# Performance work log

Hardware: AMD Instinct MI355X
Metric: run time of the kernel (lower is better)

The kernel has to match this reference:

```python
import jax, jax.numpy as jnp
import numpy as np

N = 20000        # nodes
NHID = 128       # hidden channels per head
HEADS = 4
E = 320000       # edges (before self-loops)
NLAYERS = 4
NCLASS = 40
DT, ALPHA, GAMMA = 1.0, 1.0, 1.0
NEG_SLOPE = 0.2  # PyG GATConv default


def setup_inputs() -> dict:
    key = jax.random.key(0)
    ks = jax.random.split(key, 8)
    s = 1.0 / np.sqrt(NHID)
    x = jax.random.normal(ks[0], (N, NHID), jnp.float32)
    src = jax.random.randint(ks[1], (E,), 0, N, dtype=jnp.int32)
    dst = jax.random.randint(ks[2], (E,), 0, N, dtype=jnp.int32)
    W = jax.random.normal(ks[3], (NHID, HEADS * NHID), jnp.float32) * s
    att_src = jax.random.normal(ks[4], (HEADS, NHID), jnp.float32) * s
    att_dst = jax.random.normal(ks[5], (HEADS, NHID), jnp.float32) * s
    bias = jnp.zeros((HEADS * NHID,), jnp.float32)
    Wr = jax.random.normal(ks[6], (NCLASS, NHID), jnp.float32) * s
    br = jnp.zeros((NCLASS,), jnp.float32)
    return {"x": x, "src": src, "dst": dst, "W": W, "att_src": att_src,
            "att_dst": att_dst, "bias": bias, "Wr": Wr, "br": br}


def reference(x, src, dst, W, att_src, att_dst, bias, Wr, br):
    # add self loops (PyG GATConv default)
    loop = jnp.arange(N, dtype=src.dtype)
    s_idx = jnp.concatenate([src, loop])
    d_idx = jnp.concatenate([dst, loop])

    def gat(X):
        # X: [N, NHID] -> out: [N, HEADS*NHID] (head-major, as PyG concat)
        h = (X @ W).reshape(N, HEADS, NHID)                  # [N,H,C]
        a_s = jnp.einsum('nhc,hc->nh', h, att_src)            # [N,H]
        a_d = jnp.einsum('nhc,hc->nh', h, att_dst)            # [N,H]
        e = jax.nn.leaky_relu(a_s[s_idx] + a_d[d_idx], NEG_SLOPE)  # [Etot,H]
        m = jax.ops.segment_max(e, d_idx, num_segments=N)     # scatter-softmax
        ex = jnp.exp(e - m[d_idx])
        den = jax.ops.segment_sum(ex, d_idx, num_segments=N)
        alpha = ex / den[d_idx]                               # [Etot,H]
        msg = h[s_idx] * alpha[..., None]                     # [Etot,H,C]
        out = jax.ops.segment_sum(msg, d_idx, num_segments=N)  # [N,H,C]
        return out.reshape(N, HEADS * NHID) + bias

    def step(carry, _):
        X, Y = carry
        # view(N, -1, nheads).mean(-1) on head-major [N, H*C] layout
        agg = jax.nn.elu(gat(X)).reshape(N, NHID, HEADS).mean(axis=-1)
        Y2 = Y + DT * (agg - ALPHA * Y - GAMMA * X)
        X2 = X + DT * Y2
        return (X2, Y2), (X2, Y2)

    (Xf, Yf), (Xs, Ys) = jax.lax.scan(step, (x, x), None, length=NLAYERS)
    X_all = jnp.concatenate([x[:, None], jnp.moveaxis(Xs, 0, 1)], axis=1)  # [N,L+1,C]
    Y_all = jnp.concatenate([x[:, None], jnp.moveaxis(Ys, 0, 1)], axis=1)
    out = Xf @ Wr.T + br                                     # [N, NCLASS]
    return out, X_all, Y_all
```

## Files before the change

kernel.cpp:

```cpp
#include <hip/hip_runtime.h>

typedef unsigned short u16;
typedef unsigned int u32;

#define N_NODES 20000
#define NE 320000
#define NLAYERS 4
#define NCLASS 40
#define NEG_SLOPE 0.2f
#define LSTRIDE ((NLAYERS + 1) * 128)

typedef __bf16 bf16x8 __attribute__((ext_vector_type(8)));
typedef float f32x4 __attribute__((ext_vector_type(4)));

__device__ inline u16 f2bf(float f) {
    u32 u = __float_as_uint(f);
    return (u16)((u + 0x7fffu + ((u >> 16) & 1u)) >> 16);
}
__device__ inline u32 pack2bf(float lo, float hi) {
    return (u32)f2bf(lo) | ((u32)f2bf(hi) << 16);
}

#define P1_INIT 10000
#define P1_TRANS 256
#define P1_FOLD 128
#define P1_COUNT 1250
__global__ __launch_bounds__(256) void k_pre1(
    const float* __restrict__ x, const int* __restrict__ dst,
    const float* __restrict__ W, const float* __restrict__ att_s,
    const float* __restrict__ att_d,
    u16* __restrict__ Xbf, float* __restrict__ Xall, float* __restrict__ Yall,
    u16* __restrict__ Wt, float* __restrict__ Vs, float* __restrict__ Vd,
    int* __restrict__ counts) {
    int b = blockIdx.x;
    if (b < P1_INIT) {
        int t = b * 256 + threadIdx.x;
        float v = x[t];
        Xbf[t] = f2bf(v);
        int n = t >> 7, c = t & 127;
        int ob = n * LSTRIDE + c;
        Xall[ob] = v;
        Yall[ob] = v;
    } else if (b < P1_INIT + P1_TRANS) {
        int t = (b - P1_INIT) * 256 + threadIdx.x;
        int k = t >> 9, col = t & 511;
        Wt[col * 128 + k] = f2bf(W[t]);
    } else if (b < P1_INIT + P1_TRANS + P1_FOLD) {
        int wid = ((b - P1_INIT - P1_TRANS) * 256 + threadIdx.x) >> 6;
        int lane = threadIdx.x & 63;
        int t = wid >> 2, hd = wid & 3;
        float w0 = W[t * 512 + hd * 128 + lane];
        float w1 = W[t * 512 + hd * 128 + 64 + lane];
        float s1 = w0 * att_s[hd * 128 + lane] + w1 * att_s[hd * 128 + 64 + lane];
        float s2 = w0 * att_d[hd * 128 + lane] + w1 * att_d[hd * 128 + 64 + lane];
        for (int off = 32; off; off >>= 1) {
            s1 += __shfl_xor(s1, off);
            s2 += __shfl_xor(s2, off);
        }
        if (lane == 0) {
            Vs[t * 4 + hd] = s1;
            Vd[t * 4 + hd] = s2;
        }
    } else {
        int t = (b - P1_INIT - P1_TRANS - P1_FOLD) * 256 + threadIdx.x;
        atomicAdd(&counts[dst[t]], 1);
    }
}

__global__ __launch_bounds__(1024) void k_pre2(
    const int* __restrict__ counts, int* __restrict__ indptr, int* __restrict__ cursor,
    const float* __restrict__ x, const float* __restrict__ Vs, const float* __restrict__ Vd,
    float* __restrict__ a_s, float* __restrict__ a_d) {
    if (blockIdx.x == 0) {
        __shared__ int part[1024];
        int t = threadIdx.x;
        const int CH = 20;
        int c0 = t * CH;
        int s = 0;
        for (int i = 0; i < CH; i++) {
            int idx = c0 + i;
            if (idx < N_NODES) s += counts[idx] + 1;
        }
        part[t] = s;
        __syncthreads();
        for (int off = 1; off < 1024; off <<= 1) {
            int v = 0;
            if (t >= off) v = part[t - off];
            __syncthreads();
            if (t >= off) part[t] += v;
            __syncthreads();
        }
        int ex = (t == 0) ? 0 : part[t - 1];
        for (int i = 0; i < CH; i++) {
            int idx = c0 + i;
            if (idx < N_NODES) {
                indptr[idx] = ex;
                cursor[idx] = ex;
                ex += counts[idx] + 1;
            }
        }
        if (t == 1023) indptr[N_NODES] = part[1023];
    } else {
        int wave = threadIdx.x >> 6, lane = threadIdx.x & 63;
        int n = (blockIdx.x - 1) * 16 + wave;
        const float* Xr = x + n * 128;
        float x0 = Xr[lane], x1 = Xr[64 + lane];
        f32x4 vs0 = *(const f32x4*)(Vs + lane * 4), vs1 = *(const f32x4*)(Vs + (64 + lane) * 4);
        f32x4 vd0 = *(const f32x4*)(Vd + lane * 4), vd1 = *(const f32x4*)(Vd + (64 + lane) * 4);
        f32x4 ps = x0 * vs0 + x1 * vs1;
        f32x4 pd = x0 * vd0 + x1 * vd1;
        for (int off = 32; off; off >>= 1)
            for (int c = 0; c < 4; c++) {
                ps[c] += __shfl_xor(ps[c], off);
                pd[c] += __shfl_xor(pd[c], off);
            }
        if (lane == 0) {
            *(f32x4*)(a_s + n * 4) = ps;
            *(f32x4*)(a_d + n * 4) = pd;
        }
    }
}

__global__ void k_scatter(const int* __restrict__ src, const int* __restrict__ dst,
                          int* __restrict__ cursor, int* __restrict__ esrc) {
    int t = blockIdx.x * 256 + threadIdx.x;
    if (t >= NE + N_NODES) return;
    int s, d;
    if (t < NE) { s = src[t]; d = dst[t]; }
    else { s = d = t - NE; }
    int pos = atomicAdd(&cursor[d], 1);
    esrc[pos] = s;
}

struct GatherBufs {
    int s_sh[8][2][66];
    float al_sh[8][2][66][4];
};
union LayerSmem {
    GatherBufs g;
    float aggbuf[16 * 130];
};
__global__ __launch_bounds__(512) void k_layer(
    const int* __restrict__ indptr, const int* __restrict__ esrc,
    const float* __restrict__ a_s, const float* __restrict__ a_d,
    const u16* __restrict__ XbfR, const u16* __restrict__ Wt,
    const float* __restrict__ bias,
    float* __restrict__ Xall, float* __restrict__ Yall, u16* __restrict__ XbfW,
    float* __restrict__ a_s_nxt, float* __restrict__ a_d_nxt,
    const float* __restrict__ Vs, const float* __restrict__ Vd,
    int layer, int do_logits) {
    __shared__ LayerSmem sm;
    __shared__ alignas(16) u16 As[16 * 520];
    const int t = threadIdx.x;
    const int r0 = blockIdx.x * 16;
    const int w = t >> 6, lane = t & 63;

    f32x4 acc00 = {0.f, 0.f, 0.f, 0.f}, acc01 = {0.f, 0.f, 0.f, 0.f};
    f32x4 acc10 = {0.f, 0.f, 0.f, 0.f}, acc11 = {0.f, 0.f, 0.f, 0.f};
    int d0 = r0 + w * 2;
    int st0 = indptr[d0], en0 = indptr[d0 + 1], en1 = indptr[d0 + 2];
    int st1 = en0;
    int deg0 = en0 - st0, deg1 = en1 - st1;
    f32x4 ad0 = *(const f32x4*)(a_d + d0 * 4);
    f32x4 ad1 = *(const f32x4*)(a_d + d0 * 4 + 4);

    auto prep = [&](int nd, int st, int en, f32x4 ad) {
        int j = st + lane;
        int s = 0;
        f32x4 e = {-1e30f, -1e30f, -1e30f, -1e30f};
        if (j < en) {
            s = esrc[j];
            f32x4 as = *(const f32x4*)(a_s + s * 4);
            for (int c = 0; c < 4; c++) {
                float v = as[c] + ad[c];
                e[c] = v > 0.f ? v : NEG_SLOPE * v;
            }
        }
        f32x4 mx = e;
        for (int off = 32; off; off >>= 1)
            for (int c = 0; c < 4; c++) mx[c] = fmaxf(mx[c], __shfl_xor(mx[c], off));
        f32x4 p;
        for (int c = 0; c < 4; c++) p[c] = __expf(e[c] - mx[c]);
        f32x4 den = p;
        for (int off = 32; off; off >>= 1)
            for (int c = 0; c < 4; c++) den[c] += __shfl_xor(den[c], off);
        f32x4 alpha;
        for (int c = 0; c < 4; c++) alpha[c] = p[c] * (1.f / den[c]);
        sm.g.s_sh[w][nd][lane] = s;
        *(f32x4*)sm.g.al_sh[w][nd][lane] = alpha;
        if (lane == 63) {
            sm.g.s_sh[w][nd][64] = 0;
            f32x4 z = {0.f, 0.f, 0.f, 0.f};
            *(f32x4*)sm.g.al_sh[w][nd][64] = z;
        }
    };
    auto chunk1 = [&](int nd, int cnt, f32x4& aL, f32x4& aH) {
        int sc = sm.g.s_sh[w][nd][0];
        f32x4 al = *(const f32x4*)sm.g.al_sh[w][nd][0];
        u32 xv = *(const u32*)(XbfR + sc * 128 + lane * 2);
        for (int i = 0; i < cnt; i++) {
            int sn = sm.g.s_sh[w][nd][i + 1];
            f32x4 an = *(const f32x4*)sm.g.al_sh[w][nd][i + 1];
            u32 xn = *(const u32*)(XbfR + sn * 128 + lane * 2);
            aL += al * __uint_as_float(xv << 16);
            aH += al * __uint_as_float(xv & 0xffff0000u);
            xv = xn;
            al = an;
        }
    };
    auto gen = [&](int nd, int st, int en, f32x4 ad, f32x4& aL, f32x4& aH) {
        f32x4 mx = {-1e30f, -1e30f, -1e30f, -1e30f};
        for (int j = st + lane; j < en; j += 64) {
            int s = esrc[j];
            f32x4 e = *(const f32x4*)(a_s + s * 4) + ad;
            for (int c = 0; c < 4; c++) {
                float v = e[c];
                v = v > 0.f ? v : NEG_SLOPE * v;
                mx[c] = fmaxf(mx[c], v);
            }
        }
        for (int off = 32; off; off >>= 1)
            for (int c = 0; c < 4; c++) mx[c] = fmaxf(mx[c], __shfl_xor(mx[c], off));
        f32x4 den = {0.f, 0.f, 0.f, 0.f};
        for (int j = st + lane; j < en; j += 64) {
            int s = esrc[j];
            f32x4 e = *(const f32x4*)(a_s + s * 4) + ad;
            for (int c = 0; c < 4; c++) {
                float v = e[c];
                v = v > 0.f ? v : NEG_SLOPE * v;
                den[c] += __expf(v - mx[c]);
            }
        }
        for (int off = 32; off; off >>= 1)
            for (int c = 0; c < 4; c++) den[c] += __shfl_xor(den[c], off);
        f32x4 rd;
        for (int c = 0; c < 4; c++) rd[c] = 1.f / den[c];
        for (int base = st; base < en; base += 64) {
            int cnt = min(64, en - base);
            int jj = base + lane;
            int s = 0;
            f32x4 alpha = {0.f, 0.f, 0.f, 0.f};
            if (jj < en) {
                s = esrc[jj];
                f32x4 e = *(const f32x4*)(a_s + s * 4) + ad;
                for (int c = 0; c < 4; c++) {
                    float v = e[c];
                    v = v > 0.f ? v : NEG_SLOPE * v;
                    alpha[c] = __expf(v - mx[c]) * rd[c];
                }
            }
            sm.g.s_sh[w][nd][lane] = s;
            *(f32x4*)sm.g.al_sh[w][nd][lane] = alpha;
            if (lane == 63) {
                sm.g.s_sh[w][nd][64] = 0;
                f32x4 z = {0.f, 0.f, 0.f, 0.f};
                *(f32x4*)sm.g.al_sh[w][nd][64] = z;
            }
            __builtin_amdgcn_wave_barrier();
            chunk1(nd, cnt, aL, aH);
            __builtin_amdgcn_wave_barrier();
        }
    };

    if (deg0 <= 64 && deg1 <= 64) {
        prep(0, st0, en0, ad0);
        prep(1, st1, en1, ad1);
        __builtin_amdgcn_wave_barrier();
        int cm = deg0 > deg1 ? deg0 : deg1;
        int sA = sm.g.s_sh[w][0][0], sB = sm.g.s_sh[w][1][0];
        f32x4 aA = *(const f32x4*)sm.g.al_sh[w][0][0];
        f32x4 aB = *(const f32x4*)sm.g.al_sh[w][1][0];
        u32 xA = *(const u32*)(XbfR + sA * 128 + lane * 2);
        u32 xB = *(const u32*)(XbfR + sB * 128 + lane * 2);
        for (int i = 0; i < cm; i++) {
            int sA2 = sm.g.s_sh[w][0][i + 1], sB2 = sm.g.s_sh[w][1][i + 1];
            f32x4 aA2 = *(const f32x4*)sm.g.al_sh[w][0][i + 1];
            f32x4 aB2 = *(const f32x4*)sm.g.al_sh[w][1][i + 1];
            u32 xA2 = *(const u32*)(XbfR + sA2 * 128 + lane * 2);
            u32 xB2 = *(const u32*)(XbfR + sB2 * 128 + lane * 2);
            acc00 += aA * __uint_as_float(xA << 16);
            acc01 += aA * __uint_as_float(xA & 0xffff0000u);
            acc10 += aB * __uint_as_float(xB << 16);
            acc11 += aB * __uint_as_float(xB & 0xffff0000u);
            xA = xA2; aA = aA2; xB = xB2; aB = aB2;
        }
    } else {
        gen(0, st0, en0, ad0, acc00, acc01);
        gen(1, st1, en1, ad1, acc10, acc11);
    }

    {
        u16* a0 = As + (w * 2) * 520 + lane * 2;
        u16* a1 = As + (w * 2 + 1) * 520 + lane * 2;
        for (int h = 0; h < 4; h++) {
            *(u32*)(a0 + h * 128) = pack2bf(acc00[h], acc01[h]);
            *(u32*)(a1 + h * 128) = pack2bf(acc10[h], acc11[h]);
        }
    }
    __syncthreads();

    const int h = w >> 1, colhalf = w & 1;
    const int lrow = lane & 15, quad = lane >> 4;
    f32x4 macc[4] = {};
    for (int k4 = 0; k4 < 4; k4++) {
        bf16x8 a = *(const bf16x8*)(As + lrow * 520 + h * 128 + k4 * 32 + quad * 8);
        for (int ni = 0; ni < 4; ni++) {
            bf16x8 bfrag = *(const bf16x8*)(Wt + (h * 128 + colhalf * 64 + ni * 16 + lrow) * 128 +
                                            k4 * 32 + quad * 8);
            macc[ni] = __builtin_amdgcn_mfma_f32_16x16x32_bf16(a, bfrag, macc[ni], 0, 0, 0);
        }
    }
    for (int ni = 0; ni < 4; ni++) {
        float bv = bias[h * 128 + colhalf * 64 + ni * 16 + lrow];
        for (int r = 0; r < 4; r++) {
            float v = macc[ni][r] + bv;
            v = v > 0.f ? v : __expf(v) - 1.f;
            v += __shfl_xor(v, 1);
            v += __shfl_xor(v, 2);
            if ((lrow & 3) == 0) {
                int row = quad * 4 + r;
                int cO = h * 32 + colhalf * 16 + ni * 4 + (lrow >> 2);
                sm.aggbuf[row * 130 + cO] = 0.25f * v;
            }
        }
    }
    __syncthreads();

    {
        int c = t & 127, rg = t >> 7;
        for (int rr = 0; rr < 4; rr++) {
            int row = rg * 4 + rr;
            float agg = sm.aggbuf[row * 130 + c];
            int node = r0 + row;
            int xo = node * LSTRIDE + layer * 128 + c;
            float xp = Xall[xo];
            Xall[xo + 128] = agg;
            Yall[xo + 128] = agg - xp;
            XbfW[node * 128 + c] = f2bf(agg);
        }
    }
    if (do_logits) {
        f32x4 vs0 = *(const f32x4*)(Vs + lane * 4), vs1 = *(const f32x4*)(Vs + (64 + lane) * 4);
        f32x4 vd0 = *(const f32x4*)(Vd + lane * 4), vd1 = *(const f32x4*)(Vd + (64 + lane) * 4);
        for (int rr = 0; rr < 2; rr++) {
            int row = w * 2 + rr;
            float x0 = sm.aggbuf[row * 130 + lane], x1 = sm.aggbuf[row * 130 + 64 + lane];
            f32x4 ps = x0 * vs0 + x1 * vs1;
            f32x4 pd = x0 * vd0 + x1 * vd1;
            for (int off = 32; off; off >>= 1)
                for (int c2 = 0; c2 < 4; c2++) {
                    ps[c2] += __shfl_xor(ps[c2], off);
                    pd[c2] += __shfl_xor(pd[c2], off);
                }
            if (lane == 0) {
                int node = r0 + row;
                *(f32x4*)(a_s_nxt + node * 4) = ps;
                *(f32x4*)(a_d_nxt + node * 4) = pd;
            }
        }
    }
}

__global__ __launch_bounds__(256) void k_out(const float* __restrict__ Xall,
                                             const float* __restrict__ Wr,
                                             const float* __restrict__ br,
                                             float* __restrict__ out) {
    __shared__ float Xs[4][128];
    int wave = threadIdx.x >> 6, lane = threadIdx.x & 63;
    int n = blockIdx.x * 4 + wave;
    const float* Xr = Xall + n * LSTRIDE + NLAYERS * 128;
    Xs[wave][lane] = Xr[lane];
    Xs[wave][64 + lane] = Xr[64 + lane];
    __syncthreads();
    if (lane < NCLASS) {
        float acc = 0.f;
        for (int kc = 0; kc < 32; kc++) {
            f32x4 wv = *(const f32x4*)(Wr + lane * 128 + kc * 4);
            for (int q = 0; q < 4; q++) acc += Xs[wave][kc * 4 + q] * wv[q];
        }
        out[n * NCLASS + lane] = acc + br[lane];
    }
}

extern "C" void kernel_launch(void* const* d_in, const int* in_sizes, int n_in,
                              void* d_out, int out_size, void* d_ws, size_t ws_size,
                              hipStream_t stream) {
    const float* x = (const float*)d_in[0];
    const int* src = (const int*)d_in[1];
    const int* dst = (const int*)d_in[2];
    const float* W = (const float*)d_in[3];
    const float* att_s = (const float*)d_in[4];
    const float* att_d = (const float*)d_in[5];
    const float* bias = (const float*)d_in[6];
    const float* Wr = (const float*)d_in[7];
    const float* br = (const float*)d_in[8];

    float* out = (float*)d_out;
    float* Xall = out + (size_t)N_NODES * NCLASS;
    float* Yall = Xall + (size_t)N_NODES * LSTRIDE;

    char* p = (char*)d_ws;
    auto alloc = [&](size_t bytes) -> char* {
        char* r = p;
        p += (bytes + 255) & ~(size_t)255;
        return r;
    };
    u16* XbfA = (u16*)alloc((size_t)N_NODES * 128 * 2);
    u16* XbfB = (u16*)alloc((size_t)N_NODES * 128 * 2);
    u16* Wt = (u16*)alloc(512 * 128 * 2);
    float* a_sA = (float*)alloc((size_t)N_NODES * 4 * 4);
    float* a_dA = (float*)alloc((size_t)N_NODES * 4 * 4);
    float* a_sB = (float*)alloc((size_t)N_NODES * 4 * 4);
    float* a_dB = (float*)alloc((size_t)N_NODES * 4 * 4);
    float* Vs = (float*)alloc(128 * 4 * 4);
    float* Vd = (float*)alloc(128 * 4 * 4);
    int* indptr = (int*)alloc((N_NODES + 1) * 4);
    int* cursor = (int*)alloc(N_NODES * 4);
    int* counts = (int*)alloc(N_NODES * 4);
    int* esrc = (int*)alloc((size_t)(NE + N_NODES) * 4);

    hipMemsetAsync(counts, 0, N_NODES * sizeof(int), stream);
    k_pre1<<<P1_INIT + P1_TRANS + P1_FOLD + P1_COUNT, 256, 0, stream>>>(
        x, dst, W, att_s, att_d, XbfA, Xall, Yall, Wt, Vs, Vd, counts);
    k_pre2<<<1251, 1024, 0, stream>>>(counts, indptr, cursor, x, Vs, Vd, a_sA, a_dA);
    k_scatter<<<(NE + N_NODES + 255) / 256, 256, 0, stream>>>(src, dst, cursor, esrc);

    for (int layer = 0; layer < NLAYERS; layer++) {
        const float* as_r = (layer & 1) ? a_sB : a_sA;
        const float* ad_r = (layer & 1) ? a_dB : a_dA;
        float* as_w = (layer & 1) ? a_sA : a_sB;
        float* ad_w = (layer & 1) ? a_dA : a_dB;
        const u16* xr = (layer & 1) ? XbfB : XbfA;
        u16* xw = (layer & 1) ? XbfA : XbfB;
        k_layer<<<N_NODES / 16, 512, 0, stream>>>(indptr, esrc, as_r, ad_r, xr, Wt, bias,
                                                  Xall, Yall, xw, as_w, ad_w, Vs, Vd, layer,
                                                  (layer + 1 < NLAYERS) ? 1 : 0);
    }
    k_out<<<N_NODES / 4, 256, 0, stream>>>(Xall, Wr, br, out);
}
```

Before: 482.9 us.

## Prefetch gathered neighbor rows into LDS ring with async global_load_lds pipeline

In the low-degree gather path, source-node feature rows are loaded asynchronously into a per-wave 4-slot LDS ring using global_load_lds. The loads are issued three edges ahead and paced with explicit vmcnt waits, replacing the register-level one-ahead prefetch. The goal is to keep more gather loads in flight and hide global memory latency. The padding of the index and alpha buffers grows to cover the unrolled tail. The ring shares LDS with the MMA A-tile through a union, which needs an extra block barrier. Manual vmcnt counting is fragile and adds LDS traffic.

```diff
diff --git a/kernel.cpp b/kernel.cpp
--- a/kernel.cpp
+++ b/kernel.cpp
@@ -133,12 +133,16 @@
 }
 
 struct GatherBufs {
-    int s_sh[8][2][66];
-    float al_sh[8][2][66][4];
+    int s_sh[8][2][68];
+    float al_sh[8][2][68][4];
 };
-union LayerSmem {
+union SmemA {
     GatherBufs g;
     float aggbuf[16 * 130];
+};
+union SmemB {
+    u32 ring[8][2][4][64];
+    u16 As[16 * 520];
 };
 __global__ __launch_bounds__(512) void k_layer(
     const int* __restrict__ indptr, const int* __restrict__ esrc,
@@ -149,8 +153,8 @@
     float* __restrict__ a_s_nxt, float* __restrict__ a_d_nxt,
     const float* __restrict__ Vs, const float* __restrict__ Vd,
     int layer, int do_logits) {
-    __shared__ LayerSmem sm;
-    __shared__ alignas(16) u16 As[16 * 520];
+    __shared__ alignas(16) SmemA smA;
+    __shared__ alignas(16) SmemB smB;
     const int t = threadIdx.x;
     const int r0 = blockIdx.x * 16;
     const int w = t >> 6, lane = t & 63;
@@ -186,21 +190,30 @@
             for (int c = 0; c < 4; c++) den[c] += __shfl_xor(den[c], off);
         f32x4 alpha;
         for (int c = 0; c < 4; c++) alpha[c] = p[c] * (1.f / den[c]);
-        sm.g.s_sh[w][nd][lane] = s;
-        *(f32x4*)sm.g.al_sh[w][nd][lane] = alpha;
-        if (lane == 63) {
-            sm.g.s_sh[w][nd][64] = 0;
+        smA.g.s_sh[w][nd][lane] = s;
+        *(f32x4*)smA.g.al_sh[w][nd][lane] = alpha;
+        if (lane >= 60) {
+            smA.g.s_sh[w][nd][lane + 4] = 0;
             f32x4 z = {0.f, 0.f, 0.f, 0.f};
-            *(f32x4*)sm.g.al_sh[w][nd][64] = z;
+            *(f32x4*)smA.g.al_sh[w][nd][lane + 4] = z;
         }
     };
+
+    auto issue = [&](int nd, int e, int slot) {
+        int s = smA.g.s_sh[w][nd][e];
+        const u16* gp = XbfR + s * 128 + lane * 2;
+        __builtin_amdgcn_global_load_lds(
+            (const __attribute__((address_space(1))) void*)gp,
+            (__attribute__((address_space(3))) void*)&smB.ring[w][nd][slot][0], 4, 0, 0);
+    };
+
     auto chunk1 = [&](int nd, int cnt, f32x4& aL, f32x4& aH) {
-        int sc = sm.g.s_sh[w][nd][0];
-        f32x4 al = *(const f32x4*)sm.g.al_sh[w][nd][0];
+        int sc = smA.g.s_sh[w][nd][0];
+        f32x4 al = *(const f32x4*)smA.g.al_sh[w][nd][0];
         u32 xv = *(const u32*)(XbfR + sc * 128 + lane * 2);
         for (int i = 0; i < cnt; i++) {
-            int sn = sm.g.s_sh[w][nd][i + 1];
-            f32x4 an = *(const f32x4*)sm.g.al_sh[w][nd][i + 1];
+            int sn = smA.g.s_sh[w][nd][i + 1];
+            f32x4 an = *(const f32x4*)smA.g.al_sh[w][nd][i + 1];
             u32 xn = *(const u32*)(XbfR + sn * 128 + lane * 2);
             aL += al * __uint_as_float(xv << 16);
             aH += al * __uint_as_float(xv & 0xffff0000u);
@@ -249,12 +262,12 @@
                     alpha[c] = __expf(v - mx[c]) * rd[c];
                 }
             }
-            sm.g.s_sh[w][nd][lane] = s;
-            *(f32x4*)sm.g.al_sh[w][nd][lane] = alpha;
+            smA.g.s_sh[w][nd][lane] = s;
+            *(f32x4*)smA.g.al_sh[w][nd][lane] = alpha;
             if (lane == 63) {
-                sm.g.s_sh[w][nd][64] = 0;
+                smA.g.s_sh[w][nd][64] = 0;
                 f32x4 z = {0.f, 0.f, 0.f, 0.f};
-                *(f32x4*)sm.g.al_sh[w][nd][64] = z;
+                *(f32x4*)smA.g.al_sh[w][nd][64] = z;
             }
             __builtin_amdgcn_wave_barrier();
             chunk1(nd, cnt, aL, aH);
@@ -267,34 +280,46 @@
         prep(1, st1, en1, ad1);
         __builtin_amdgcn_wave_barrier();
         int cm = deg0 > deg1 ? deg0 : deg1;
-        int sA = sm.g.s_sh[w][0][0], sB = sm.g.s_sh[w][1][0];
-        f32x4 aA = *(const f32x4*)sm.g.al_sh[w][0][0];
-        f32x4 aB = *(const f32x4*)sm.g.al_sh[w][1][0];
-        u32 xA = *(const u32*)(XbfR + sA * 128 + lane * 2);
-        u32 xB = *(const u32*)(XbfR + sB * 128 + lane * 2);
-        for (int i = 0; i < cm; i++) {
-            int sA2 = sm.g.s_sh[w][0][i + 1], sB2 = sm.g.s_sh[w][1][i + 1];
-            f32x4 aA2 = *(const f32x4*)sm.g.al_sh[w][0][i + 1];
-            f32x4 aB2 = *(const f32x4*)sm.g.al_sh[w][1][i + 1];
-            u32 xA2 = *(const u32*)(XbfR + sA2 * 128 + lane * 2);
-            u32 xB2 = *(const u32*)(XbfR + sB2 * 128 + lane * 2);
-            acc00 += aA * __uint_as_float(xA << 16);
-            acc01 += aA * __uint_as_float(xA & 0xffff0000u);
-            acc10 += aB * __uint_as_float(xB << 16);
-            acc11 += aB * __uint_as_float(xB & 0xffff0000u);
-            xA = xA2; aA = aA2; xB = xB2; aB = aB2;
-        }
+        int cmp = (cm + 3) & ~3;
+        issue(0, 0, 0); issue(1, 0, 0);
+        issue(0, 1, 1); issue(1, 1, 1);
+        issue(0, 2, 2); issue(1, 2, 2);
+        for (int i = 0; i < cmp; i += 4) {
+#define GSTEP(K, SL, SL3)                                                  \
+    {                                                                      \
+        f32x4 aA = *(const f32x4*)smA.g.al_sh[w][0][i + (K)];              \
+        f32x4 aB = *(const f32x4*)smA.g.al_sh[w][1][i + (K)];              \
+        asm volatile("s_waitcnt vmcnt(4)" ::: "memory");                   \
+        __builtin_amdgcn_sched_barrier(0);                                 \
+        u32 xA = smB.ring[w][0][SL][lane];                                 \
+        u32 xB = smB.ring[w][1][SL][lane];                                 \
+        acc00 += aA * __uint_as_float(xA << 16);                           \
+        acc01 += aA * __uint_as_float(xA & 0xffff0000u);                   \
+        acc10 += aB * __uint_as_float(xB << 16);                           \
+        acc11 += aB * __uint_as_float(xB & 0xffff0000u);                   \
+        issue(0, i + (K) + 3, SL3);                                        \
+        issue(1, i + (K) + 3, SL3);                                        \
+    }
+            GSTEP(0, 0, 3)
+            GSTEP(1, 1, 0)
+            GSTEP(2, 2, 1)
+            GSTEP(3, 3, 2)
+#undef GSTEP
+        }
+        asm volatile("s_waitcnt vmcnt(0)" ::: "memory");
+        __builtin_amdgcn_sched_barrier(0);
     } else {
         gen(0, st0, en0, ad0, acc00, acc01);
         gen(1, st1, en1, ad1, acc10, acc11);
     }
+    __syncthreads();
 
     {
-        u16* a0 = As + (w * 2) * 520 + lane * 2;
-        u16* a1 = As + (w * 2 + 1) * 520 + lane * 2;
-        for (int h = 0; h < 4; h++) {
-            *(u32*)(a0 + h * 128) = pack2bf(acc00[h], acc01[h]);
-            *(u32*)(a1 + h * 128) = pack2bf(acc10[h], acc11[h]);
+        u16* a0 = smB.As + (w * 2) * 520 + lane * 2;
+        u16* a1 = smB.As + (w * 2 + 1) * 520 + lane * 2;
+        for (int h2 = 0; h2 < 4; h2++) {
+            *(u32*)(a0 + h2 * 128) = pack2bf(acc00[h2], acc01[h2]);
+            *(u32*)(a1 + h2 * 128) = pack2bf(acc10[h2], acc11[h2]);
         }
     }
     __syncthreads();
@@ -303,7 +328,7 @@
     const int lrow = lane & 15, quad = lane >> 4;
     f32x4 macc[4] = {};
     for (int k4 = 0; k4 < 4; k4++) {
-        bf16x8 a = *(const bf16x8*)(As + lrow * 520 + h * 128 + k4 * 32 + quad * 8);
+        bf16x8 a = *(const bf16x8*)(smB.As + lrow * 520 + h * 128 + k4 * 32 + quad * 8);
         for (int ni = 0; ni < 4; ni++) {
             bf16x8 bfrag = *(const bf16x8*)(Wt + (h * 128 + colhalf * 64 + ni * 16 + lrow) * 128 +
                                             k4 * 32 + quad * 8);
@@ -320,7 +345,7 @@
             if ((lrow & 3) == 0) {
                 int row = quad * 4 + r;
                 int cO = h * 32 + colhalf * 16 + ni * 4 + (lrow >> 2);
-                sm.aggbuf[row * 130 + cO] = 0.25f * v;
+                smA.aggbuf[row * 130 + cO] = 0.25f * v;
             }
         }
     }
@@ -330,7 +355,7 @@
         int c = t & 127, rg = t >> 7;
         for (int rr = 0; rr < 4; rr++) {
             int row = rg * 4 + rr;
-            float agg = sm.aggbuf[row * 130 + c];
+            float agg = smA.aggbuf[row * 130 + c];
             int node = r0 + row;
             int xo = node * LSTRIDE + layer * 128 + c;
             float xp = Xall[xo];
@@ -344,7 +369,7 @@
         f32x4 vd0 = *(const f32x4*)(Vd + lane * 4), vd1 = *(const f32x4*)(Vd + (64 + lane) * 4);
         for (int rr = 0; rr < 2; rr++) {
             int row = w * 2 + rr;
-            float x0 = sm.aggbuf[row * 130 + lane], x1 = sm.aggbuf[row * 130 + 64 + lane];
+            float x0 = smA.aggbuf[row * 130 + lane], x1 = smA.aggbuf[row * 130 + 64 + lane];
             f32x4 ps = x0 * vs0 + x1 * vs1;
             f32x4 pd = x0 * vd0 + x1 * vd1;
             for (int off = 32; off; off >>= 1)
```

Result: slower. 500.0 us (+3.5%).
